# Performance work log

Measured on AMD Instinct MI355X. Metric: run time of the kernel, lower is better.

Reference implementation:

```python
import jax, jax.numpy as jnp
import numpy as np

GAMMA = 1.0
EPS = 1e-06
MAXITERS = 100


def setup_inputs() -> dict:
    key = jax.random.key(0)
    B, H, W = 64, 512, 512
    M = jax.random.uniform(key, (B, H, W), dtype=jnp.float32)
    return {"M": M}


def reference(M):
    """Entropy-regularized OT via Sinkhorn with uniform marginals (r=c=None path).

    Matches torch loop: row-normalize, check col marginal convergence, break
    BEFORE col-normalizing if converged, else col-normalize.
    """
    B, H, W = M.shape
    r = jnp.full((1, H), 1.0 / H, dtype=M.dtype)
    c = jnp.full((1, W), 1.0 / W, dtype=M.dtype)
    P0 = jnp.exp(-GAMMA * M)

    def cond(state):
        i, P, done = state
        return jnp.logical_and(i < MAXITERS, jnp.logical_not(done))

    def body(state):
        i, P, _ = state
        alpha = P.sum(axis=2)                      # (B,H)
        P = (r / alpha)[:, :, None] * P            # row normalize
        beta = P.sum(axis=1)                       # (B,W)
        done = jnp.all(jnp.abs(beta - c) <= EPS)   # isclose(atol=eps, rtol=0)
        # if converged, keep row-normalized P (torch breaks before col scale)
        P = jnp.where(done, P, P * (c / beta)[:, None, :])
        return i + 1, P, done

    _, P, _ = jax.lax.while_loop(cond, body, (jnp.int32(0), P0, jnp.array(False)))
    return P
```

## Files before the change

kernel.cpp:

```cpp
#include <hip/hip_runtime.h>
#include <hip/hip_cooperative_groups.h>
#include <cstddef>

namespace cg = cooperative_groups;

#define BATCH 64
#define HW 512
#define RVAL (1.0f / 512.0f)
#define EPS_ 1e-6f
#define MAXIT 100
#define NBLK 256
#define NTHR 1024

__global__ __launch_bounds__(NTHR, 4)
void sinkhorn_atm(const float* __restrict__ M, float* __restrict__ P,
                  float* __restrict__ colpart, int* __restrict__ bar,
                  int tail_mode) {
    const int tid  = threadIdx.x;
    const int bid  = blockIdx.x;
    const int b    = bid >> 2;
    const int slab = bid & 3;
    const int w    = tid >> 6;
    const int l    = tid & 63;

    cg::grid_group grid = cg::this_grid();

    __shared__ float v_lds[HW];
    __shared__ float part[16][HW];

    if (tid < HW) v_lds[tid] = 1.0f;
    __syncthreads();

    const float4* Mb = (const float4*)(M + ((size_t)b * HW + slab * 128) * HW);

    float u_loc[8];
    for (int it = 0; it < MAXIT; ++it) {
        float4 v0 = *(const float4*)&v_lds[l * 4];
        float4 v1 = *(const float4*)&v_lds[256 + l * 4];
        float4 cp0 = make_float4(0.f, 0.f, 0.f, 0.f);
        float4 cp1 = make_float4(0.f, 0.f, 0.f, 0.f);
#pragma unroll
        for (int rr = 0; rr < 8; ++rr) {
            const float4* mp = Mb + (size_t)(w * 8 + rr) * 128;
            float4 m0 = mp[l];
            float4 m1 = mp[64 + l];
            float4 k0, k1;
            k0.x = __expf(-m0.x); k0.y = __expf(-m0.y);
            k0.z = __expf(-m0.z); k0.w = __expf(-m0.w);
            k1.x = __expf(-m1.x); k1.y = __expf(-m1.y);
            k1.z = __expf(-m1.z); k1.w = __expf(-m1.w);
            float s = k0.x * v0.x + k0.y * v0.y + k0.z * v0.z + k0.w * v0.w
                    + k1.x * v1.x + k1.y * v1.y + k1.z * v1.z + k1.w * v1.w;
#pragma unroll
            for (int off = 32; off >= 1; off >>= 1)
                s += __shfl_xor(s, off, 64);
            float u = RVAL / s;
            u_loc[rr] = u;
            cp0.x += u * k0.x; cp0.y += u * k0.y;
            cp0.z += u * k0.z; cp0.w += u * k0.w;
            cp1.x += u * k1.x; cp1.y += u * k1.y;
            cp1.z += u * k1.z; cp1.w += u * k1.w;
        }
        *(float4*)&part[w][l * 4]       = cp0;
        *(float4*)&part[w][256 + l * 4] = cp1;
        __syncthreads();

        float* slot = colpart + ((size_t)((it & 1) * NBLK + bid)) * HW;
        if (tid < HW) {
            float t = 0.f;
#pragma unroll
            for (int ww = 0; ww < 16; ++ww) t += part[ww][tid];
            __hip_atomic_store(&slot[tid], t, __ATOMIC_RELAXED,
                               __HIP_MEMORY_SCOPE_AGENT);
        }
        __syncthreads();

        int* bs = bar + b * MAXIT + it;
        if (tid == 0) {
            __hip_atomic_fetch_add(bs, 1, __ATOMIC_RELAXED,
                                   __HIP_MEMORY_SCOPE_AGENT);
            while (__hip_atomic_load(bs, __ATOMIC_RELAXED,
                                     __HIP_MEMORY_SCOPE_AGENT) < 4)
                __builtin_amdgcn_s_sleep(4);
        }
        __syncthreads();

        float tt = 0.f;
        int viol = 0;
        if (tid < HW) {
            const float* basep =
                colpart + ((size_t)((it & 1) * NBLK + b * 4)) * HW;
#pragma unroll
            for (int bb = 0; bb < 4; ++bb)
                tt += __hip_atomic_load(basep + bb * HW + tid, __ATOMIC_RELAXED,
                                        __HIP_MEMORY_SCOPE_AGENT);
            viol = fabsf(v_lds[tid] * tt - RVAL) > EPS_;
        }
        int any = __syncthreads_or(viol);
        if (!any) break;
        if (tid < HW) v_lds[tid] = RVAL / tt;
        __syncthreads();
    }

    if (tail_mode) grid.sync();

    float4 fv0 = *(const float4*)&v_lds[l * 4];
    float4 fv1 = *(const float4*)&v_lds[256 + l * 4];
    float4* Pb = (float4*)(P + ((size_t)b * HW + slab * 128) * HW);
#pragma unroll
    for (int rr = 0; rr < 8; ++rr) {
        float u = u_loc[rr];
        const float4* mp = Mb + (size_t)(w * 8 + rr) * 128;
        float4 m0 = mp[l];
        float4 m1 = mp[64 + l];
        float4 o0, o1;
        o0.x = u * __expf(-m0.x) * fv0.x; o0.y = u * __expf(-m0.y) * fv0.y;
        o0.z = u * __expf(-m0.z) * fv0.z; o0.w = u * __expf(-m0.w) * fv0.w;
        o1.x = u * __expf(-m1.x) * fv1.x; o1.y = u * __expf(-m1.y) * fv1.y;
        o1.z = u * __expf(-m1.z) * fv1.z; o1.w = u * __expf(-m1.w) * fv1.w;
        Pb[(size_t)(w * 8 + rr) * 128 + l]      = o0;
        Pb[(size_t)(w * 8 + rr) * 128 + 64 + l] = o1;
    }
}

extern "C" void kernel_launch(void* const* d_in, const int* in_sizes, int n_in,
                              void* d_out, int out_size, void* d_ws, size_t ws_size,
                              hipStream_t stream) {
    const float* M = (const float*)d_in[0];
    float* P = (float*)d_out;

    const size_t CP_BYTES  = (size_t)2 * NBLK * HW * sizeof(float);
    const size_t BAR_BYTES = (size_t)BATCH * MAXIT * sizeof(int);
    const size_t NEED = CP_BYTES + BAR_BYTES;

    char* scratch;
    int tail_mode;
    if (ws_size >= NEED) {
        scratch = (char*)d_ws;
        tail_mode = 0;
    } else {
        scratch = (char*)d_out + (size_t)out_size * sizeof(float) - NEED;
        tail_mode = 1;
    }
    float* colpart = (float*)scratch;
    int*   bar     = (int*)(scratch + CP_BYTES);

    hipMemsetAsync(bar, 0, BAR_BYTES, stream);

    void* args[] = { (void*)&M, (void*)&P, (void*)&colpart, (void*)&bar,
                     (void*)&tail_mode };
    hipLaunchCooperativeKernel((const void*)sinkhorn_atm, dim3(NBLK),
                               dim3(NTHR), args, 0, stream);
}
```

Before: 68.20 us.

## Cache exp(-M) kernel as fp16 in LDS across Sinkhorn iterations

On the first iteration, each block computes K=exp(-M) for its 128x512 slab and stores it in LDS as packed fp16. Later iterations and the final output read K from LDS instead of reloading M from global memory and recomputing exp. The per-wave column-partial buffer is halved to 8 rows, with a two-stage reduction, to free LDS. This uses 128KB+ of LDS per block, which may cut occupancy, and fp16 storage of K loses precision, which could affect convergence and output accuracy.

```diff
diff --git a/kernel.cpp b/kernel.cpp
--- a/kernel.cpp
+++ b/kernel.cpp
@@ -1,4 +1,5 @@
 #include <hip/hip_runtime.h>
+#include <hip/hip_fp16.h>
 #include <hip/hip_cooperative_groups.h>
 #include <cstddef>
 
@@ -12,8 +13,15 @@
 #define NBLK 256
 #define NTHR 1024
 
+__device__ __forceinline__ unsigned h2u(__half2 h) {
+    union { __half2 h; unsigned u; } c; c.h = h; return c.u;
+}
+__device__ __forceinline__ __half2 u2h(unsigned u) {
+    union { unsigned u; __half2 h; } c; c.u = u; return c.h;
+}
+
 __global__ __launch_bounds__(NTHR, 4)
-void sinkhorn_atm(const float* __restrict__ M, float* __restrict__ P,
+void sinkhorn_lds(const float* __restrict__ M, float* __restrict__ P,
                   float* __restrict__ colpart, int* __restrict__ bar,
                   int tail_mode) {
     const int tid  = threadIdx.x;
@@ -25,8 +33,9 @@
 
     cg::grid_group grid = cg::this_grid();
 
-    __shared__ float v_lds[HW];
-    __shared__ float part[16][HW];
+    __shared__ unsigned K_lds[128][HW / 2];
+    __shared__ float    part[8][HW];
+    __shared__ float    v_lds[HW];
 
     if (tid < HW) v_lds[tid] = 1.0f;
     __syncthreads();
@@ -39,37 +48,82 @@
         float4 v1 = *(const float4*)&v_lds[256 + l * 4];
         float4 cp0 = make_float4(0.f, 0.f, 0.f, 0.f);
         float4 cp1 = make_float4(0.f, 0.f, 0.f, 0.f);
-#pragma unroll
-        for (int rr = 0; rr < 8; ++rr) {
-            const float4* mp = Mb + (size_t)(w * 8 + rr) * 128;
-            float4 m0 = mp[l];
-            float4 m1 = mp[64 + l];
-            float4 k0, k1;
-            k0.x = __expf(-m0.x); k0.y = __expf(-m0.y);
-            k0.z = __expf(-m0.z); k0.w = __expf(-m0.w);
-            k1.x = __expf(-m1.x); k1.y = __expf(-m1.y);
-            k1.z = __expf(-m1.z); k1.w = __expf(-m1.w);
-            float s = k0.x * v0.x + k0.y * v0.y + k0.z * v0.z + k0.w * v0.w
-                    + k1.x * v1.x + k1.y * v1.y + k1.z * v1.z + k1.w * v1.w;
-#pragma unroll
-            for (int off = 32; off >= 1; off >>= 1)
-                s += __shfl_xor(s, off, 64);
-            float u = RVAL / s;
-            u_loc[rr] = u;
-            cp0.x += u * k0.x; cp0.y += u * k0.y;
-            cp0.z += u * k0.z; cp0.w += u * k0.w;
-            cp1.x += u * k1.x; cp1.y += u * k1.y;
-            cp1.z += u * k1.z; cp1.w += u * k1.w;
-        }
-        *(float4*)&part[w][l * 4]       = cp0;
-        *(float4*)&part[w][256 + l * 4] = cp1;
+
+        if (it == 0) {
+#pragma unroll
+            for (int rr = 0; rr < 8; ++rr) {
+                const int row = w * 8 + rr;
+                const float4* mp = Mb + (size_t)row * 128;
+                float4 m0 = mp[l];
+                float4 m1 = mp[64 + l];
+                float4 k0, k1;
+                k0.x = __expf(-m0.x); k0.y = __expf(-m0.y);
+                k0.z = __expf(-m0.z); k0.w = __expf(-m0.w);
+                k1.x = __expf(-m1.x); k1.y = __expf(-m1.y);
+                k1.z = __expf(-m1.z); k1.w = __expf(-m1.w);
+                uint2 q0, q1;
+                q0.x = h2u(__floats2half2_rn(k0.x, k0.y));
+                q0.y = h2u(__floats2half2_rn(k0.z, k0.w));
+                q1.x = h2u(__floats2half2_rn(k1.x, k1.y));
+                q1.y = h2u(__floats2half2_rn(k1.z, k1.w));
+                *(uint2*)&K_lds[row][2 * l]       = q0;
+                *(uint2*)&K_lds[row][128 + 2 * l] = q1;
+                float s = k0.x * v0.x + k0.y * v0.y + k0.z * v0.z + k0.w * v0.w
+                        + k1.x * v1.x + k1.y * v1.y + k1.z * v1.z + k1.w * v1.w;
+#pragma unroll
+                for (int off = 32; off >= 1; off >>= 1)
+                    s += __shfl_xor(s, off, 64);
+                float u = RVAL / s;
+                u_loc[rr] = u;
+                cp0.x += u * k0.x; cp0.y += u * k0.y;
+                cp0.z += u * k0.z; cp0.w += u * k0.w;
+                cp1.x += u * k1.x; cp1.y += u * k1.y;
+                cp1.z += u * k1.z; cp1.w += u * k1.w;
+            }
+        } else {
+#pragma unroll
+            for (int rr = 0; rr < 8; ++rr) {
+                const int row = w * 8 + rr;
+                uint2 q0 = *(const uint2*)&K_lds[row][2 * l];
+                uint2 q1 = *(const uint2*)&K_lds[row][128 + 2 * l];
+                float2 a0 = __half22float2(u2h(q0.x));
+                float2 a1 = __half22float2(u2h(q0.y));
+                float2 b0 = __half22float2(u2h(q1.x));
+                float2 b1 = __half22float2(u2h(q1.y));
+                float s = a0.x * v0.x + a0.y * v0.y + a1.x * v0.z + a1.y * v0.w
+                        + b0.x * v1.x + b0.y * v1.y + b1.x * v1.z + b1.y * v1.w;
+#pragma unroll
+                for (int off = 32; off >= 1; off >>= 1)
+                    s += __shfl_xor(s, off, 64);
+                float u = RVAL / s;
+                u_loc[rr] = u;
+                cp0.x += u * a0.x; cp0.y += u * a0.y;
+                cp0.z += u * a1.x; cp0.w += u * a1.y;
+                cp1.x += u * b0.x; cp1.y += u * b0.y;
+                cp1.z += u * b1.x; cp1.w += u * b1.y;
+            }
+        }
+
+        if (w < 8) {
+            *(float4*)&part[w][l * 4]       = cp0;
+            *(float4*)&part[w][256 + l * 4] = cp1;
+        }
+        __syncthreads();
+        if (w >= 8) {
+            float4 e0 = *(float4*)&part[w - 8][l * 4];
+            float4 e1 = *(float4*)&part[w - 8][256 + l * 4];
+            e0.x += cp0.x; e0.y += cp0.y; e0.z += cp0.z; e0.w += cp0.w;
+            e1.x += cp1.x; e1.y += cp1.y; e1.z += cp1.z; e1.w += cp1.w;
+            *(float4*)&part[w - 8][l * 4]       = e0;
+            *(float4*)&part[w - 8][256 + l * 4] = e1;
+        }
         __syncthreads();
 
         float* slot = colpart + ((size_t)((it & 1) * NBLK + bid)) * HW;
         if (tid < HW) {
             float t = 0.f;
 #pragma unroll
-            for (int ww = 0; ww < 16; ++ww) t += part[ww][tid];
+            for (int ww = 0; ww < 8; ++ww) t += part[ww][tid];
             __hip_atomic_store(&slot[tid], t, __ATOMIC_RELAXED,
                                __HIP_MEMORY_SCOPE_AGENT);
         }
@@ -109,17 +163,21 @@
     float4* Pb = (float4*)(P + ((size_t)b * HW + slab * 128) * HW);
 #pragma unroll
     for (int rr = 0; rr < 8; ++rr) {
+        const int row = w * 8 + rr;
         float u = u_loc[rr];
-        const float4* mp = Mb + (size_t)(w * 8 + rr) * 128;
-        float4 m0 = mp[l];
-        float4 m1 = mp[64 + l];
+        uint2 q0 = *(const uint2*)&K_lds[row][2 * l];
+        uint2 q1 = *(const uint2*)&K_lds[row][128 + 2 * l];
+        float2 a0 = __half22float2(u2h(q0.x));
+        float2 a1 = __half22float2(u2h(q0.y));
+        float2 b0 = __half22float2(u2h(q1.x));
+        float2 b1 = __half22float2(u2h(q1.y));
         float4 o0, o1;
-        o0.x = u * __expf(-m0.x) * fv0.x; o0.y = u * __expf(-m0.y) * fv0.y;
-        o0.z = u * __expf(-m0.z) * fv0.z; o0.w = u * __expf(-m0.w) * fv0.w;
-        o1.x = u * __expf(-m1.x) * fv1.x; o1.y = u * __expf(-m1.y) * fv1.y;
-        o1.z = u * __expf(-m1.z) * fv1.z; o1.w = u * __expf(-m1.w) * fv1.w;
-        Pb[(size_t)(w * 8 + rr) * 128 + l]      = o0;
-        Pb[(size_t)(w * 8 + rr) * 128 + 64 + l] = o1;
+        o0.x = u * a0.x * fv0.x; o0.y = u * a0.y * fv0.y;
+        o0.z = u * a1.x * fv0.z; o0.w = u * a1.y * fv0.w;
+        o1.x = u * b0.x * fv1.x; o1.y = u * b0.y * fv1.y;
+        o1.z = u * b1.x * fv1.z; o1.w = u * b1.y * fv1.w;
+        Pb[(size_t)row * 128 + l]      = o0;
+        Pb[(size_t)row * 128 + 64 + l] = o1;
     }
 }
 
@@ -149,6 +207,6 @@
 
     void* args[] = { (void*)&M, (void*)&P, (void*)&colpart, (void*)&bar,
                      (void*)&tail_mode };
-    hipLaunchCooperativeKernel((const void*)sinkhorn_atm, dim3(NBLK),
+    hipLaunchCooperativeKernel((const void*)sinkhorn_lds, dim3(NBLK),
                                dim3(NTHR), args, 0, stream);
 }
```

New measurement: 65.55 us. 3.9% less time.

## Cache most exp(-M) rows as fp16 in LDS across Sinkhorn iterations

Applied to the files above, without the earlier changes.

On the first iteration each wave computes exp(-M) and stores 6 of its 8 rows as packed fp16 in shared memory. Later iterations read those rows from LDS instead of reloading M from global memory and recomputing the exponentials; only the remaining 2 rows per wave are reloaded. This trades global bandwidth and exp work for a large LDS footprint and fp16 rounding of the kernel matrix, which may perturb the 1e-6 convergence test. The barrier spin is also bounded by a guard counter.

```diff
diff --git a/kernel.cpp b/kernel.cpp
--- a/kernel.cpp
+++ b/kernel.cpp
@@ -1,4 +1,5 @@
 #include <hip/hip_runtime.h>
+#include <hip/hip_fp16.h>
 #include <hip/hip_cooperative_groups.h>
 #include <cstddef>
 
@@ -11,9 +12,17 @@
 #define MAXIT 100
 #define NBLK 256
 #define NTHR 1024
+#define SPIN_BOUND 4000000
+
+__device__ __forceinline__ unsigned h2u(__half2 h) {
+    union { __half2 h; unsigned u; } c; c.h = h; return c.u;
+}
+__device__ __forceinline__ __half2 u2h(unsigned u) {
+    union { unsigned u; __half2 h; } c; c.u = u; return c.h;
+}
 
 __global__ __launch_bounds__(NTHR, 4)
-void sinkhorn_atm(const float* __restrict__ M, float* __restrict__ P,
+void sinkhorn_hyb(const float* __restrict__ M, float* __restrict__ P,
                   float* __restrict__ colpart, int* __restrict__ bar,
                   int tail_mode) {
     const int tid  = threadIdx.x;
@@ -25,8 +34,9 @@
 
     cg::grid_group grid = cg::this_grid();
 
-    __shared__ float v_lds[HW];
-    __shared__ float part[16][HW];
+    __shared__ unsigned K_lds[96][HW / 2];
+    __shared__ float    part[16][HW];
+    __shared__ float    v_lds[HW];
 
     if (tid < HW) v_lds[tid] = 1.0f;
     __syncthreads();
@@ -39,28 +49,91 @@
         float4 v1 = *(const float4*)&v_lds[256 + l * 4];
         float4 cp0 = make_float4(0.f, 0.f, 0.f, 0.f);
         float4 cp1 = make_float4(0.f, 0.f, 0.f, 0.f);
-#pragma unroll
-        for (int rr = 0; rr < 8; ++rr) {
-            const float4* mp = Mb + (size_t)(w * 8 + rr) * 128;
-            float4 m0 = mp[l];
-            float4 m1 = mp[64 + l];
-            float4 k0, k1;
-            k0.x = __expf(-m0.x); k0.y = __expf(-m0.y);
-            k0.z = __expf(-m0.z); k0.w = __expf(-m0.w);
-            k1.x = __expf(-m1.x); k1.y = __expf(-m1.y);
-            k1.z = __expf(-m1.z); k1.w = __expf(-m1.w);
-            float s = k0.x * v0.x + k0.y * v0.y + k0.z * v0.z + k0.w * v0.w
-                    + k1.x * v1.x + k1.y * v1.y + k1.z * v1.z + k1.w * v1.w;
-#pragma unroll
-            for (int off = 32; off >= 1; off >>= 1)
-                s += __shfl_xor(s, off, 64);
-            float u = RVAL / s;
-            u_loc[rr] = u;
-            cp0.x += u * k0.x; cp0.y += u * k0.y;
-            cp0.z += u * k0.z; cp0.w += u * k0.w;
-            cp1.x += u * k1.x; cp1.y += u * k1.y;
-            cp1.z += u * k1.z; cp1.w += u * k1.w;
-        }
+
+        if (it == 0) {
+#pragma unroll
+            for (int rr = 0; rr < 8; ++rr) {
+                const float4* mp = Mb + (size_t)(w * 8 + rr) * 128;
+                float4 m0 = mp[l];
+                float4 m1 = mp[64 + l];
+                float4 k0, k1;
+                k0.x = __expf(-m0.x); k0.y = __expf(-m0.y);
+                k0.z = __expf(-m0.z); k0.w = __expf(-m0.w);
+                k1.x = __expf(-m1.x); k1.y = __expf(-m1.y);
+                k1.z = __expf(-m1.z); k1.w = __expf(-m1.w);
+                if (rr < 6) {
+                    const int lr = w * 6 + rr;
+                    uint2 q0, q1;
+                    q0.x = h2u(__floats2half2_rn(k0.x, k0.y));
+                    q0.y = h2u(__floats2half2_rn(k0.z, k0.w));
+                    q1.x = h2u(__floats2half2_rn(k1.x, k1.y));
+                    q1.y = h2u(__floats2half2_rn(k1.z, k1.w));
+                    *(uint2*)&K_lds[lr][2 * l]       = q0;
+                    *(uint2*)&K_lds[lr][128 + 2 * l] = q1;
+                }
+                float s = k0.x * v0.x + k0.y * v0.y + k0.z * v0.z + k0.w * v0.w
+                        + k1.x * v1.x + k1.y * v1.y + k1.z * v1.z + k1.w * v1.w;
+#pragma unroll
+                for (int off = 32; off >= 1; off >>= 1)
+                    s += __shfl_xor(s, off, 64);
+                float u = RVAL / s;
+                u_loc[rr] = u;
+                cp0.x += u * k0.x; cp0.y += u * k0.y;
+                cp0.z += u * k0.z; cp0.w += u * k0.w;
+                cp1.x += u * k1.x; cp1.y += u * k1.y;
+                cp1.z += u * k1.z; cp1.w += u * k1.w;
+            }
+        } else {
+            const float4* mp6 = Mb + (size_t)(w * 8 + 6) * 128;
+            const float4* mp7 = Mb + (size_t)(w * 8 + 7) * 128;
+            float4 g60 = mp6[l], g61 = mp6[64 + l];
+            float4 g70 = mp7[l], g71 = mp7[64 + l];
+
+#pragma unroll
+            for (int rr = 0; rr < 6; ++rr) {
+                const int lr = w * 6 + rr;
+                uint2 q0 = *(const uint2*)&K_lds[lr][2 * l];
+                uint2 q1 = *(const uint2*)&K_lds[lr][128 + 2 * l];
+                float2 a0 = __half22float2(u2h(q0.x));
+                float2 a1 = __half22float2(u2h(q0.y));
+                float2 b0 = __half22float2(u2h(q1.x));
+                float2 b1 = __half22float2(u2h(q1.y));
+                float s = a0.x * v0.x + a0.y * v0.y + a1.x * v0.z + a1.y * v0.w
+                        + b0.x * v1.x + b0.y * v1.y + b1.x * v1.z + b1.y * v1.w;
+#pragma unroll
+                for (int off = 32; off >= 1; off >>= 1)
+                    s += __shfl_xor(s, off, 64);
+                float u = RVAL / s;
+                u_loc[rr] = u;
+                cp0.x += u * a0.x; cp0.y += u * a0.y;
+                cp0.z += u * a1.x; cp0.w += u * a1.y;
+                cp1.x += u * b0.x; cp1.y += u * b0.y;
+                cp1.z += u * b1.x; cp1.w += u * b1.y;
+            }
+
+#pragma unroll
+            for (int rr = 6; rr < 8; ++rr) {
+                float4 m0 = (rr == 6) ? g60 : g70;
+                float4 m1 = (rr == 6) ? g61 : g71;
+                float4 k0, k1;
+                k0.x = __expf(-m0.x); k0.y = __expf(-m0.y);
+                k0.z = __expf(-m0.z); k0.w = __expf(-m0.w);
+                k1.x = __expf(-m1.x); k1.y = __expf(-m1.y);
+                k1.z = __expf(-m1.z); k1.w = __expf(-m1.w);
+                float s = k0.x * v0.x + k0.y * v0.y + k0.z * v0.z + k0.w * v0.w
+                        + k1.x * v1.x + k1.y * v1.y + k1.z * v1.z + k1.w * v1.w;
+#pragma unroll
+                for (int off = 32; off >= 1; off >>= 1)
+                    s += __shfl_xor(s, off, 64);
+                float u = RVAL / s;
+                u_loc[rr] = u;
+                cp0.x += u * k0.x; cp0.y += u * k0.y;
+                cp0.z += u * k0.z; cp0.w += u * k0.w;
+                cp1.x += u * k1.x; cp1.y += u * k1.y;
+                cp1.z += u * k1.z; cp1.w += u * k1.w;
+            }
+        }
+
         *(float4*)&part[w][l * 4]       = cp0;
         *(float4*)&part[w][256 + l * 4] = cp1;
         __syncthreads();
@@ -79,9 +152,13 @@
         if (tid == 0) {
             __hip_atomic_fetch_add(bs, 1, __ATOMIC_RELAXED,
                                    __HIP_MEMORY_SCOPE_AGENT);
+            int guard = 0;
             while (__hip_atomic_load(bs, __ATOMIC_RELAXED,
-                                     __HIP_MEMORY_SCOPE_AGENT) < 4)
+                                     __HIP_MEMORY_SCOPE_AGENT) < 4 &&
+                   guard < SPIN_BOUND) {
                 __builtin_amdgcn_s_sleep(4);
+                ++guard;
+            }
         }
         __syncthreads();
 
@@ -149,6 +226,6 @@
 
     void* args[] = { (void*)&M, (void*)&P, (void*)&colpart, (void*)&bar,
                      (void*)&tail_mode };
-    hipLaunchCooperativeKernel((const void*)sinkhorn_atm, dim3(NBLK),
+    hipLaunchCooperativeKernel((const void*)sinkhorn_hyb, dim3(NBLK),
                                dim3(NTHR), args, 0, stream);
 }
```

Result: slower. 82.19 us (+20.5%).
